# Performance work log

Measured on AMD Instinct MI355X. Metric: run time of the kernel, lower is better.

## Reference

```python
import math
import jax, jax.numpy as jnp
import numpy as np

D_HIDDEN, D_MODEL, SEQ_LEN = 2048, 4096, 4096
R_MIN, R_MAX, MAX_PHASE = 0.0, 1.0, 6.28


def setup_inputs() -> dict:
    key = jax.random.key(0)
    ks = jax.random.split(key, 8)
    # nu_log / theta_log per the LRU stable-ring init
    u1 = jax.random.uniform(ks[0], (D_HIDDEN,))
    nu_log = jnp.log(-0.5 * jnp.log(u1 * (R_MAX ** 2 - R_MIN ** 2) + R_MIN ** 2))
    u2 = jax.random.uniform(ks[1], (D_HIDDEN,))
    theta_log = jnp.log(MAX_PHASE * u2)
    diag_lambda = jnp.exp(-jnp.exp(nu_log) + 1j * jnp.exp(theta_log))
    gamma_log = jnp.log(jnp.sqrt(1.0 - jnp.abs(diag_lambda) ** 2))
    B_re = jax.random.normal(ks[2], (D_HIDDEN, D_MODEL)) / math.sqrt(2 * D_MODEL)
    B_im = jax.random.normal(ks[3], (D_HIDDEN, D_MODEL)) / math.sqrt(2 * D_MODEL)
    C_re = jax.random.normal(ks[4], (D_MODEL, D_HIDDEN)) / math.sqrt(D_HIDDEN)
    C_im = jax.random.normal(ks[5], (D_MODEL, D_HIDDEN)) / math.sqrt(D_HIDDEN)
    D = jax.random.normal(ks[6], (D_MODEL,))
    inputs = jax.random.normal(ks[7], (SEQ_LEN, D_MODEL), dtype=jnp.float32)
    return {
        "inputs": inputs,
        "nu_log": nu_log,
        "theta_log": theta_log,
        "gamma_log": gamma_log,
        "B_re": B_re,
        "B_im": B_im,
        "C_re": C_re,
        "C_im": C_im,
        "D": D,
    }


def reference(inputs, nu_log, theta_log, gamma_log, B_re, B_im, C_re, C_im, D):
    x = inputs.astype(jnp.complex64)
    # Diagonal complex recurrence matrix
    diag_lambda = jnp.exp(-jnp.exp(nu_log) + 1j * jnp.exp(theta_log))  # (H,)
    B_norm = (B_re + 1j * B_im) * jnp.exp(gamma_log)[:, None]          # (H, D)
    Bu = jnp.einsum('hd,td->th', B_norm, x)                            # (T, H)
    Lam = jnp.broadcast_to(diag_lambda, Bu.shape)                       # (T, H)

    # h_t = lambda * h_{t-1} + Bu_t  via log-depth associative scan
    def op(a, b):
        return (a[0] * b[0], b[0] * a[1] + b[1])

    _, hidden = jax.lax.associative_scan(op, (Lam, Bu))                 # (T, H)

    C = C_re + 1j * C_im                                                # (D, H)
    outputs = jnp.matmul(hidden, C.T).real + inputs * D                 # (T, D)
    return outputs.astype(jnp.float32)
```

## Files before the change

kernel.cpp:

```cpp
#include <hip/hip_runtime.h>
#include <hip/hip_bf16.h>

typedef unsigned short u16;
typedef float f32x4 __attribute__((ext_vector_type(4)));
typedef __bf16 bf16x8 __attribute__((ext_vector_type(8)));

constexpr int TSEQ = 4096;
constexpr int DMOD = 4096;
constexpr int HID  = 2048;
constexpr int HID2 = 4096;
constexpr int NCH  = 64;
constexpr int CHL  = 64;

__device__ __forceinline__ u16 f2bf(float f) {
  unsigned u = __builtin_bit_cast(unsigned, f);
  u += 0x7fffu + ((u >> 16) & 1u);
  return (u16)(u >> 16);
}
__device__ __forceinline__ float bf2f(u16 u) {
  return __builtin_bit_cast(float, (unsigned)u << 16);
}
__device__ __forceinline__ unsigned pack2(float a, float b) {
  return (unsigned)f2bf(a) | ((unsigned)f2bf(b) << 16);
}
__device__ __forceinline__ void load_lds16(const u16* g, u16* l) {
  __builtin_amdgcn_global_load_lds((const __attribute__((address_space(1))) void*)g,
                                   (__attribute__((address_space(3))) void*)l,
                                   16, 0, 0);
}
__device__ __forceinline__ unsigned lds_addr(const u16* p) {
  return (unsigned)(uintptr_t)(const __attribute__((address_space(3))) u16*)p;
}

__global__ __launch_bounds__(256) void k_lambda(const float* __restrict__ nu_log,
                                                const float* __restrict__ theta_log,
                                                float* __restrict__ lam_re, float* __restrict__ lam_im,
                                                float* __restrict__ lamL_re, float* __restrict__ lamL_im) {
  int h = blockIdx.x * 256 + threadIdx.x;
  if (h >= HID) return;
  float nu = expf(nu_log[h]);
  float th = expf(theta_log[h]);
  float mag = expf(-nu);
  float lr = mag * cosf(th), li = mag * sinf(th);
  lam_re[h] = lr; lam_im[h] = li;
  float pr = lr, pi = li;
#pragma unroll
  for (int i = 0; i < 6; ++i) {
    float nr = pr * pr - pi * pi;
    float ni = 2.f * pr * pi;
    pr = nr; pi = ni;
  }
  lamL_re[h] = pr; lamL_im[h] = pi;
}

__global__ __launch_bounds__(256) void k_cast_x(const float* __restrict__ x, u16* __restrict__ xb) {
  size_t i = ((size_t)blockIdx.x * 256 + threadIdx.x) * 4;
  float4 v = *reinterpret_cast<const float4*>(x + i);
  uint2 o;
  o.x = pack2(v.x, v.y);
  o.y = pack2(v.z, v.w);
  *reinterpret_cast<uint2*>(xb + i) = o;
}

__global__ __launch_bounds__(256) void k_make_bcat(const float* __restrict__ Bre, const float* __restrict__ Bim,
                                                   const float* __restrict__ gamma_log, u16* __restrict__ Bcat) {
  int idx = blockIdx.x * 256 + threadIdx.x;
  int h  = idx / (DMOD / 4);
  int dv = (idx % (DMOD / 4)) * 4;
  float g = expf(gamma_log[h]);
  float4 r  = *reinterpret_cast<const float4*>(Bre + (size_t)h * DMOD + dv);
  float4 im = *reinterpret_cast<const float4*>(Bim + (size_t)h * DMOD + dv);
  uint2 orr; orr.x = pack2(r.x * g, r.y * g); orr.y = pack2(r.z * g, r.w * g);
  *reinterpret_cast<uint2*>(Bcat + (size_t)h * DMOD + dv) = orr;
  uint2 oim; oim.x = pack2(im.x * g, im.y * g); oim.y = pack2(im.z * g, im.w * g);
  *reinterpret_cast<uint2*>(Bcat + (size_t)(h + HID) * DMOD + dv) = oim;
}

__global__ __launch_bounds__(256) void k_make_ccat(const float* __restrict__ Cre, const float* __restrict__ Cim,
                                                   u16* __restrict__ Ccat) {
  int idx = blockIdx.x * 256 + threadIdx.x;
  int d  = idx / (HID / 4);
  int hv = (idx % (HID / 4)) * 4;
  float4 r  = *reinterpret_cast<const float4*>(Cre + (size_t)d * HID + hv);
  float4 im = *reinterpret_cast<const float4*>(Cim + (size_t)d * HID + hv);
  uint2 orr; orr.x = pack2(r.x, r.y); orr.y = pack2(r.z, r.w);
  *reinterpret_cast<uint2*>(Ccat + (size_t)d * HID2 + hv) = orr;
  uint2 oim; oim.x = pack2(-im.x, -im.y); oim.y = pack2(-im.z, -im.w);
  *reinterpret_cast<uint2*>(Ccat + (size_t)d * HID2 + HID + hv) = oim;
}

#define DSR(d, a, IMM) asm volatile("ds_read_b128 %0, %1 offset:" IMM : "=v"(d) : "v"(a))

#define RD_A(B, O0, O1, O2, O3) do { \
  DSR(af[0][0], aAk0[B], O0); DSR(af[0][1], aAk1[B], O0); \
  DSR(af[1][0], aAk0[B], O1); DSR(af[1][1], aAk1[B], O1); \
  DSR(af[2][0], aAk0[B], O2); DSR(af[2][1], aAk1[B], O2); \
  DSR(af[3][0], aAk0[B], O3); DSR(af[3][1], aAk1[B], O3); } while (0)

#define RD_B(B, DST, O0, O1) do { \
  DSR(DST[0][0], aBk0[B], O0); DSR(DST[0][1], aBk1[B], O0); \
  DSR(DST[1][0], aBk0[B], O1); DSR(DST[1][1], aBk1[B], O1); } while (0)

#define STAGE_A(b, h, kb) do { const u16* _s = stA + (size_t)(h) * 128 * 4096 + (kb); \
  load_lds16(_s, dA[b][h]); load_lds16(_s + 64 * 4096, dA[b][h] + 4096); } while (0)
#define STAGE_B(b, h, kb) do { const u16* _s = stB + (size_t)(h) * 128 * 4096 + (kb); \
  load_lds16(_s, dB[b][h]); load_lds16(_s + 64 * 4096, dB[b][h] + 4096); } while (0)

#define MMQ(MB, NB, BF) do { \
  _Pragma("unroll") for (int k = 0; k < 2; ++k) { \
  _Pragma("unroll") for (int m = 0; m < 4; ++m) { \
  _Pragma("unroll") for (int n = 0; n < 2; ++n) { \
    acc[(MB)+m][(NB)+n] = __builtin_amdgcn_mfma_f32_16x16x32_bf16(af[m][k], BF[n][k], acc[(MB)+m][(NB)+n], 0, 0, 0); } } } } while (0)

#define MID() do { __builtin_amdgcn_s_barrier(); \
  asm volatile("s_waitcnt lgkmcnt(0)"); \
  __builtin_amdgcn_sched_barrier(0); \
  __builtin_amdgcn_s_setprio(1); } while (0)
#define ENDP() do { __builtin_amdgcn_s_setprio(0); \
  __builtin_amdgcn_s_barrier(); } while (0)
#define ENDPV() do { __builtin_amdgcn_s_setprio(0); \
  asm volatile("s_waitcnt vmcnt(4)"); \
  __builtin_amdgcn_s_barrier(); } while (0)

template <bool EPI>
__global__ __launch_bounds__(512, 2) void gemm8(const u16* __restrict__ A, const u16* __restrict__ Bt,
                                                void* __restrict__ Cout,
                                                const float* __restrict__ resid,
                                                const float* __restrict__ dvec) {
  constexpr int K = 4096, N = 4096;
  constexpr int NI = (K / 64) / 2;
  __shared__ __align__(16) u16 L[65536];

  int nwg = gridDim.x;
  int wg = blockIdx.x;
  wg = (wg & 7) * (nwg >> 3) + (wg >> 3);
  int bm = (wg >> 4) << 8;
  int bn = (wg & 15) << 8;

  int tid = threadIdx.x;
  int lane = tid & 63;
  int wave = tid >> 6;
  int wm = wave >> 2, wn = wave & 3;
  int l15 = lane & 15, g = lane >> 4;

  unsigned offk0 = (unsigned)(((unsigned)g << 4) ^ ((unsigned)(lane & 7) << 4));
  unsigned offk1 = offk0 ^ 64u;
  unsigned aAk0[2], aAk1[2], aBk0[2], aBk1[2];
#pragma unroll
  for (int b = 0; b < 2; ++b) {
    unsigned ab = lds_addr(&L[b * 32768 + wm * 8192 + l15 * 64]);
    aAk0[b] = ab + offk0; aAk1[b] = ab + offk1;
    unsigned bb = lds_addr(&L[b * 32768 + 16384 + (wn >> 1) * 8192 + (wn & 1) * 4096 + l15 * 64]);
    aBk0[b] = bb + offk0; aBk1[b] = bb + offk1;
  }

  int trow = tid >> 3;
  int tchk = ((tid & 7) ^ (trow & 7)) << 3;
  const u16* stA = A  + (size_t)(bm + trow) * K + tchk;
  const u16* stB = Bt + (size_t)(bn + trow) * K + tchk;
  u16* dA[2][2]; u16* dB[2][2];
#pragma unroll
  for (int b = 0; b < 2; ++b)
#pragma unroll
    for (int h = 0; h < 2; ++h) {
      dA[b][h] = &L[b * 32768 + h * 8192 + tid * 8];
      dB[b][h] = &L[b * 32768 + 16384 + h * 8192 + tid * 8];
    }

  bf16x8 af[4][2], b0[2][2], b1[2][2];
  f32x4 acc[8][4];
#pragma unroll
  for (int i = 0; i < 8; ++i)
#pragma unroll
    for (int n = 0; n < 4; ++n) acc[i][n] = (f32x4){0.f, 0.f, 0.f, 0.f};

  STAGE_B(0, 0, 0);  STAGE_A(0, 0, 0);
  STAGE_B(0, 1, 0);  STAGE_A(0, 1, 0);
  STAGE_B(1, 0, 64); STAGE_A(1, 0, 64);
  asm volatile("s_waitcnt vmcnt(4)");
  __builtin_amdgcn_s_barrier();

#pragma unroll 1
  for (int j = 0; j < NI; ++j) {
    int kb1 = ((2 * j + 1) << 6) & (K - 1);
    int kb2 = ((2 * j + 2) << 6) & (K - 1);
    int kb3 = ((2 * j + 3) << 6) & (K - 1);
    RD_A(0, "0", "2048", "4096", "6144");
    RD_B(0, b0, "0", "2048");
    STAGE_B(1, 1, kb1);
    MID(); MMQ(0, 0, b0); ENDP();
    RD_B(0, b1, "4096", "6144");
    STAGE_A(1, 1, kb1);
    MID(); MMQ(0, 2, b1); ENDP();
    RD_A(0, "8192", "10240", "12288", "14336");
    STAGE_B(0, 0, kb2);
    MID(); MMQ(4, 2, b1); ENDP();
    STAGE_A(0, 0, kb2);
    MID(); MMQ(4, 0, b0); ENDPV();
    RD_A(1, "0", "2048", "4096", "6144");
    RD_B(1, b0, "0", "2048");
    STAGE_B(0, 1, kb2);
    MID(); MMQ(0, 0, b0); ENDP();
    RD_B(1, b1, "4096", "6144");
    STAGE_A(0, 1, kb2);
    MID(); MMQ(0, 2, b1); ENDP();
    RD_A(1, "8192", "10240", "12288", "14336");
    STAGE_B(1, 0, kb3);
    MID(); MMQ(4, 2, b1); ENDP();
    STAGE_A(1, 0, kb3);
    MID(); MMQ(4, 0, b0); ENDPV();
  }

  int crow = bm + wm * 128 + (g << 2);
  int ccol = bn + wn * 64 + l15;
#pragma unroll
  for (int mi = 0; mi < 8; ++mi)
#pragma unroll
    for (int ni = 0; ni < 4; ++ni)
#pragma unroll
      for (int jj = 0; jj < 4; ++jj) {
        int row = crow + mi * 16 + jj;
        int col = ccol + ni * 16;
        float v = acc[mi][ni][jj];
        if constexpr (EPI) {
          v += resid[(size_t)row * N + col] * dvec[col];
          ((float*)Cout)[(size_t)row * N + col] = v;
        } else {
          ((u16*)Cout)[(size_t)row * N + col] = f2bf(v);
        }
      }
}

__global__ __launch_bounds__(256) void s_chunk_end(const u16* __restrict__ Bu,
                                                   const float* __restrict__ lam_re,
                                                   const float* __restrict__ lam_im,
                                                   float* __restrict__ E) {
  int t = blockIdx.x * 256 + threadIdx.x;
  int hq = t & (HID / 4 - 1);
  int c  = t >> 9;
  int h0 = hq << 2;
  float4 lr = *reinterpret_cast<const float4*>(lam_re + h0);
  float4 li = *reinterpret_cast<const float4*>(lam_im + h0);
  float sr[4] = {0.f, 0.f, 0.f, 0.f}, si[4] = {0.f, 0.f, 0.f, 0.f};
  const float lrv[4] = {lr.x, lr.y, lr.z, lr.w};
  const float liv[4] = {li.x, li.y, li.z, li.w};
  const u16* base = Bu + (size_t)c * CHL * HID2 + h0;
#pragma unroll 8
  for (int i = 0; i < CHL; ++i) {
    ushort4 vre = *reinterpret_cast<const ushort4*>(base + (size_t)i * HID2);
    ushort4 vim = *reinterpret_cast<const ushort4*>(base + (size_t)i * HID2 + HID);
    float br[4] = {bf2f(vre.x), bf2f(vre.y), bf2f(vre.z), bf2f(vre.w)};
    float bi[4] = {bf2f(vim.x), bf2f(vim.y), bf2f(vim.z), bf2f(vim.w)};
#pragma unroll
    for (int q = 0; q < 4; ++q) {
      float nr = lrv[q] * sr[q] - liv[q] * si[q] + br[q];
      float ni = lrv[q] * si[q] + liv[q] * sr[q] + bi[q];
      sr[q] = nr; si[q] = ni;
    }
  }
  *reinterpret_cast<float4*>(E + (size_t)c * HID + h0) = (float4){sr[0], sr[1], sr[2], sr[3]};
  *reinterpret_cast<float4*>(E + (size_t)NCH * HID + (size_t)c * HID + h0) = (float4){si[0], si[1], si[2], si[3]};
}

__global__ __launch_bounds__(256) void s_prefix(const float* __restrict__ lamL_re,
                                                const float* __restrict__ lamL_im,
                                                const float* __restrict__ E,
                                                float* __restrict__ P) {
  int h = blockIdx.x * 256 + threadIdx.x;
  if (h >= HID) return;
  float plr = lamL_re[h], pli = lamL_im[h];
  float pr = 0.f, pi = 0.f;
#pragma unroll
  for (int c = 0; c < NCH; ++c) {
    P[(size_t)c * HID + h] = pr;
    P[(size_t)NCH * HID + (size_t)c * HID + h] = pi;
    float er = E[(size_t)c * HID + h];
    float ei = E[(size_t)NCH * HID + (size_t)c * HID + h];
    float nr = plr * pr - pli * pi + er;
    float ni = plr * pi + pli * pr + ei;
    pr = nr; pi = ni;
  }
}

__global__ __launch_bounds__(256) void s_expand(const u16* __restrict__ Bu,
                                                const float* __restrict__ lam_re,
                                                const float* __restrict__ lam_im,
                                                const float* __restrict__ P,
                                                u16* __restrict__ A2) {
  int t = blockIdx.x * 256 + threadIdx.x;
  int hq = t & (HID / 4 - 1);
  int c  = t >> 9;
  int h0 = hq << 2;
  float4 lr = *reinterpret_cast<const float4*>(lam_re + h0);
  float4 li = *reinterpret_cast<const float4*>(lam_im + h0);
  const float lrv[4] = {lr.x, lr.y, lr.z, lr.w};
  const float liv[4] = {li.x, li.y, li.z, li.w};
  float4 p0 = *reinterpret_cast<const float4*>(P + (size_t)c * HID + h0);
  float4 p1 = *reinterpret_cast<const float4*>(P + (size_t)NCH * HID + (size_t)c * HID + h0);
  float sr[4] = {p0.x, p0.y, p0.z, p0.w}, si[4] = {p1.x, p1.y, p1.z, p1.w};
  const u16* base = Bu + (size_t)c * CHL * HID2 + h0;
  u16* ob = A2 + (size_t)c * CHL * HID2 + h0;
#pragma unroll 8
  for (int i = 0; i < CHL; ++i) {
    ushort4 vre = *reinterpret_cast<const ushort4*>(base + (size_t)i * HID2);
    ushort4 vim = *reinterpret_cast<const ushort4*>(base + (size_t)i * HID2 + HID);
    float br[4] = {bf2f(vre.x), bf2f(vre.y), bf2f(vre.z), bf2f(vre.w)};
    float bi[4] = {bf2f(vim.x), bf2f(vim.y), bf2f(vim.z), bf2f(vim.w)};
#pragma unroll
    for (int q = 0; q < 4; ++q) {
      float nr = lrv[q] * sr[q] - liv[q] * si[q] + br[q];
      float ni = lrv[q] * si[q] + liv[q] * sr[q] + bi[q];
      sr[q] = nr; si[q] = ni;
    }
    ushort4 ore = {f2bf(sr[0]), f2bf(sr[1]), f2bf(sr[2]), f2bf(sr[3])};
    ushort4 oim = {f2bf(si[0]), f2bf(si[1]), f2bf(si[2]), f2bf(si[3])};
    *reinterpret_cast<ushort4*>(ob + (size_t)i * HID2) = ore;
    *reinterpret_cast<ushort4*>(ob + (size_t)i * HID2 + HID) = oim;
  }
}

extern "C" void kernel_launch(void* const* d_in, const int* in_sizes, int n_in,
                              void* d_out, int out_size, void* d_ws, size_t ws_size,
                              hipStream_t stream) {
  const float* inputs    = (const float*)d_in[0];
  const float* nu_log    = (const float*)d_in[1];
  const float* theta_log = (const float*)d_in[2];
  const float* gamma_log = (const float*)d_in[3];
  const float* B_re      = (const float*)d_in[4];
  const float* B_im      = (const float*)d_in[5];
  const float* C_re      = (const float*)d_in[6];
  const float* C_im      = (const float*)d_in[7];
  const float* Dvec      = (const float*)d_in[8];

  char* w = (char*)d_ws;
  u16* xb     = (u16*)w;
  u16* Bcat   = (u16*)(w + (size_t)33554432);
  float* lam_re  = (float*)(w + (size_t)67108864);
  float* lam_im  = lam_re + HID;
  float* lamL_re = lam_im + HID;
  float* lamL_im = lamL_re + HID;
  float* E       = lamL_im + HID;
  float* P       = E + (size_t)NCH * HID * 2;

  u16* Bu    = (u16*)d_out;
  float* out = (float*)d_out;

  k_lambda<<<dim3(HID / 256), dim3(256), 0, stream>>>(nu_log, theta_log, lam_re, lam_im, lamL_re, lamL_im);
  k_cast_x<<<dim3((TSEQ * DMOD / 4) / 256), dim3(256), 0, stream>>>(inputs, xb);
  k_make_bcat<<<dim3((HID * DMOD / 4) / 256), dim3(256), 0, stream>>>(B_re, B_im, gamma_log, Bcat);

  gemm8<false><<<dim3((TSEQ / 256) * (HID2 / 256)), dim3(512), 0, stream>>>(
      xb, Bcat, (void*)Bu, nullptr, nullptr);

  s_chunk_end<<<dim3(NCH * HID / 4 / 256), dim3(256), 0, stream>>>(Bu, lam_re, lam_im, E);
  s_prefix<<<dim3(HID / 256), dim3(256), 0, stream>>>(lamL_re, lamL_im, E, P);
  s_expand<<<dim3(NCH * HID / 4 / 256), dim3(256), 0, stream>>>(Bu, lam_re, lam_im, P, xb );

  k_make_ccat<<<dim3((DMOD * HID / 4) / 256), dim3(256), 0, stream>>>(C_re, C_im, Bcat );

  gemm8<true><<<dim3((TSEQ / 256) * (DMOD / 256)), dim3(512), 0, stream>>>(
      xb , Bcat , (void*)out, inputs, Dvec);
}
```

Before: 478.8 us.

## Shorten scan chunks, widen scan parallelism, and double-buffer GEMM A fragments

```diff
diff --git a/kernel.cpp b/kernel.cpp
--- a/kernel.cpp
+++ b/kernel.cpp
@@ -9,8 +9,8 @@
 constexpr int DMOD = 4096;
 constexpr int HID  = 2048;
 constexpr int HID2 = 4096;
-constexpr int NCH  = 64;
-constexpr int CHL  = 64;
+constexpr int NCH  = 128;
+constexpr int CHL  = 32;
 
 __device__ __forceinline__ u16 f2bf(float f) {
   unsigned u = __builtin_bit_cast(unsigned, f);
@@ -45,7 +45,7 @@
   lam_re[h] = lr; lam_im[h] = li;
   float pr = lr, pi = li;
 #pragma unroll
-  for (int i = 0; i < 6; ++i) {
+  for (int i = 0; i < 5; ++i) {
     float nr = pr * pr - pi * pi;
     float ni = 2.f * pr * pi;
     pr = nr; pi = ni;
@@ -91,11 +91,11 @@
 
 #define DSR(d, a, IMM) asm volatile("ds_read_b128 %0, %1 offset:" IMM : "=v"(d) : "v"(a))
 
-#define RD_A(B, O0, O1, O2, O3) do { \
-  DSR(af[0][0], aAk0[B], O0); DSR(af[0][1], aAk1[B], O0); \
-  DSR(af[1][0], aAk0[B], O1); DSR(af[1][1], aAk1[B], O1); \
-  DSR(af[2][0], aAk0[B], O2); DSR(af[2][1], aAk1[B], O2); \
-  DSR(af[3][0], aAk0[B], O3); DSR(af[3][1], aAk1[B], O3); } while (0)
+#define RD_A(AF, B, O0, O1, O2, O3) do { \
+  DSR(AF[0][0], aAk0[B], O0); DSR(AF[0][1], aAk1[B], O0); \
+  DSR(AF[1][0], aAk0[B], O1); DSR(AF[1][1], aAk1[B], O1); \
+  DSR(AF[2][0], aAk0[B], O2); DSR(AF[2][1], aAk1[B], O2); \
+  DSR(AF[3][0], aAk0[B], O3); DSR(AF[3][1], aAk1[B], O3); } while (0)
 
 #define RD_B(B, DST, O0, O1) do { \
   DSR(DST[0][0], aBk0[B], O0); DSR(DST[0][1], aBk1[B], O0); \
@@ -106,14 +106,14 @@
 #define STAGE_B(b, h, kb) do { const u16* _s = stB + (size_t)(h) * 128 * 4096 + (kb); \
   load_lds16(_s, dB[b][h]); load_lds16(_s + 64 * 4096, dB[b][h] + 4096); } while (0)
 
-#define MMQ(MB, NB, BF) do { \
+#define MMQ(AF, MB, NB, BF) do { \
   _Pragma("unroll") for (int k = 0; k < 2; ++k) { \
   _Pragma("unroll") for (int m = 0; m < 4; ++m) { \
   _Pragma("unroll") for (int n = 0; n < 2; ++n) { \
-    acc[(MB)+m][(NB)+n] = __builtin_amdgcn_mfma_f32_16x16x32_bf16(af[m][k], BF[n][k], acc[(MB)+m][(NB)+n], 0, 0, 0); } } } } while (0)
-
-#define MID() do { __builtin_amdgcn_s_barrier(); \
-  asm volatile("s_waitcnt lgkmcnt(0)"); \
+    acc[(MB)+m][(NB)+n] = __builtin_amdgcn_mfma_f32_16x16x32_bf16(AF[m][k], BF[n][k], acc[(MB)+m][(NB)+n], 0, 0, 0); } } } } while (0)
+
+#define MIDN(CNT) do { __builtin_amdgcn_s_barrier(); \
+  asm volatile("s_waitcnt lgkmcnt(" CNT ")"); \
   __builtin_amdgcn_sched_barrier(0); \
   __builtin_amdgcn_s_setprio(1); } while (0)
 #define ENDP() do { __builtin_amdgcn_s_setprio(0); \
@@ -167,7 +167,7 @@
       dB[b][h] = &L[b * 32768 + 16384 + h * 8192 + tid * 8];
     }
 
-  bf16x8 af[4][2], b0[2][2], b1[2][2];
+  bf16x8 af1[4][2], af2[4][2], b0[2][2], b1[2][2];
   f32x4 acc[8][4];
 #pragma unroll
   for (int i = 0; i < 8; ++i)
@@ -185,30 +185,30 @@
     int kb1 = ((2 * j + 1) << 6) & (K - 1);
     int kb2 = ((2 * j + 2) << 6) & (K - 1);
     int kb3 = ((2 * j + 3) << 6) & (K - 1);
-    RD_A(0, "0", "2048", "4096", "6144");
+    RD_A(af1, 0, "0", "2048", "4096", "6144");
     RD_B(0, b0, "0", "2048");
+    RD_B(0, b1, "4096", "6144");
     STAGE_B(1, 1, kb1);
-    MID(); MMQ(0, 0, b0); ENDP();
-    RD_B(0, b1, "4096", "6144");
+    MIDN("4"); MMQ(af1, 0, 0, b0); ENDP();
+    RD_A(af2, 0, "8192", "10240", "12288", "14336");
     STAGE_A(1, 1, kb1);
-    MID(); MMQ(0, 2, b1); ENDP();
-    RD_A(0, "8192", "10240", "12288", "14336");
+    MIDN("8"); MMQ(af1, 0, 2, b1); ENDP();
     STAGE_B(0, 0, kb2);
-    MID(); MMQ(4, 2, b1); ENDP();
+    MIDN("0"); MMQ(af2, 4, 2, b1); ENDP();
     STAGE_A(0, 0, kb2);
-    MID(); MMQ(4, 0, b0); ENDPV();
-    RD_A(1, "0", "2048", "4096", "6144");
+    MIDN("0"); MMQ(af2, 4, 0, b0); ENDPV();
+    RD_A(af1, 1, "0", "2048", "4096", "6144");
     RD_B(1, b0, "0", "2048");
+    RD_B(1, b1, "4096", "6144");
     STAGE_B(0, 1, kb2);
-    MID(); MMQ(0, 0, b0); ENDP();
-    RD_B(1, b1, "4096", "6144");
+    MIDN("4"); MMQ(af1, 0, 0, b0); ENDP();
+    RD_A(af2, 1, "8192", "10240", "12288", "14336");
     STAGE_A(0, 1, kb2);
-    MID(); MMQ(0, 2, b1); ENDP();
-    RD_A(1, "8192", "10240", "12288", "14336");
+    MIDN("8"); MMQ(af1, 0, 2, b1); ENDP();
     STAGE_B(1, 0, kb3);
-    MID(); MMQ(4, 2, b1); ENDP();
+    MIDN("0"); MMQ(af2, 4, 2, b1); ENDP();
     STAGE_A(1, 0, kb3);
-    MID(); MMQ(4, 0, b0); ENDPV();
+    MIDN("0"); MMQ(af2, 4, 0, b0); ENDPV();
   }
 
   int crow = bm + wm * 128 + (g << 2);
@@ -236,30 +236,25 @@
                                                    const float* __restrict__ lam_im,
                                                    float* __restrict__ E) {
   int t = blockIdx.x * 256 + threadIdx.x;
-  int hq = t & (HID / 4 - 1);
-  int c  = t >> 9;
-  int h0 = hq << 2;
-  float4 lr = *reinterpret_cast<const float4*>(lam_re + h0);
-  float4 li = *reinterpret_cast<const float4*>(lam_im + h0);
-  float sr[4] = {0.f, 0.f, 0.f, 0.f}, si[4] = {0.f, 0.f, 0.f, 0.f};
-  const float lrv[4] = {lr.x, lr.y, lr.z, lr.w};
-  const float liv[4] = {li.x, li.y, li.z, li.w};
+  int hp = t & (HID / 2 - 1);
+  int c  = t >> 10;
+  int h0 = hp << 1;
+  float2 lr = *reinterpret_cast<const float2*>(lam_re + h0);
+  float2 li = *reinterpret_cast<const float2*>(lam_im + h0);
+  float sr0 = 0.f, si0 = 0.f, sr1 = 0.f, si1 = 0.f;
   const u16* base = Bu + (size_t)c * CHL * HID2 + h0;
 #pragma unroll 8
   for (int i = 0; i < CHL; ++i) {
-    ushort4 vre = *reinterpret_cast<const ushort4*>(base + (size_t)i * HID2);
-    ushort4 vim = *reinterpret_cast<const ushort4*>(base + (size_t)i * HID2 + HID);
-    float br[4] = {bf2f(vre.x), bf2f(vre.y), bf2f(vre.z), bf2f(vre.w)};
-    float bi[4] = {bf2f(vim.x), bf2f(vim.y), bf2f(vim.z), bf2f(vim.w)};
-#pragma unroll
-    for (int q = 0; q < 4; ++q) {
-      float nr = lrv[q] * sr[q] - liv[q] * si[q] + br[q];
-      float ni = lrv[q] * si[q] + liv[q] * sr[q] + bi[q];
-      sr[q] = nr; si[q] = ni;
-    }
-  }
-  *reinterpret_cast<float4*>(E + (size_t)c * HID + h0) = (float4){sr[0], sr[1], sr[2], sr[3]};
-  *reinterpret_cast<float4*>(E + (size_t)NCH * HID + (size_t)c * HID + h0) = (float4){si[0], si[1], si[2], si[3]};
+    ushort2 vre = *reinterpret_cast<const ushort2*>(base + (size_t)i * HID2);
+    ushort2 vim = *reinterpret_cast<const ushort2*>(base + (size_t)i * HID2 + HID);
+    float nr0 = lr.x * sr0 - li.x * si0 + bf2f(vre.x);
+    float ni0 = lr.x * si0 + li.x * sr0 + bf2f(vim.x);
+    float nr1 = lr.y * sr1 - li.y * si1 + bf2f(vre.y);
+    float ni1 = lr.y * si1 + li.y * sr1 + bf2f(vim.y);
+    sr0 = nr0; si0 = ni0; sr1 = nr1; si1 = ni1;
+  }
+  *reinterpret_cast<float2*>(E + (size_t)c * HID + h0) = (float2){sr0, sr1};
+  *reinterpret_cast<float2*>(E + (size_t)NCH * HID + (size_t)c * HID + h0) = (float2){si0, si1};
 }
 
 __global__ __launch_bounds__(256) void s_prefix(const float* __restrict__ lamL_re,
@@ -270,7 +265,7 @@
   if (h >= HID) return;
   float plr = lamL_re[h], pli = lamL_im[h];
   float pr = 0.f, pi = 0.f;
-#pragma unroll
+#pragma unroll 8
   for (int c = 0; c < NCH; ++c) {
     P[(size_t)c * HID + h] = pr;
     P[(size_t)NCH * HID + (size_t)c * HID + h] = pi;
@@ -288,34 +283,27 @@
                                                 const float* __restrict__ P,
                                                 u16* __restrict__ A2) {
   int t = blockIdx.x * 256 + threadIdx.x;
-  int hq = t & (HID / 4 - 1);
-  int c  = t >> 9;
-  int h0 = hq << 2;
-  float4 lr = *reinterpret_cast<const float4*>(lam_re + h0);
-  float4 li = *reinterpret_cast<const float4*>(lam_im + h0);
-  const float lrv[4] = {lr.x, lr.y, lr.z, lr.w};
-  const float liv[4] = {li.x, li.y, li.z, li.w};
-  float4 p0 = *reinterpret_cast<const float4*>(P + (size_t)c * HID + h0);
-  float4 p1 = *reinterpret_cast<const float4*>(P + (size_t)NCH * HID + (size_t)c * HID + h0);
-  float sr[4] = {p0.x, p0.y, p0.z, p0.w}, si[4] = {p1.x, p1.y, p1.z, p1.w};
+  int hp = t & (HID / 2 - 1);
+  int c  = t >> 10;
+  int h0 = hp << 1;
+  float2 lr = *reinterpret_cast<const float2*>(lam_re + h0);
+  float2 li = *reinterpret_cast<const float2*>(lam_im + h0);
+  float2 p0 = *reinterpret_cast<const float2*>(P + (size_t)c * HID + h0);
+  float2 p1 = *reinterpret_cast<const float2*>(P + (size_t)NCH * HID + (size_t)c * HID + h0);
+  float sr0 = p0.x, sr1 = p0.y, si0 = p1.x, si1 = p1.y;
   const u16* base = Bu + (size_t)c * CHL * HID2 + h0;
   u16* ob = A2 + (size_t)c * CHL * HID2 + h0;
 #pragma unroll 8
   for (int i = 0; i < CHL; ++i) {
-    ushort4 vre = *reinterpret_cast<const ushort4*>(base + (size_t)i * HID2);
-    ushort4 vim = *reinterpret_cast<const ushort4*>(base + (size_t)i * HID2 + HID);
-    float br[4] = {bf2f(vre.x), bf2f(vre.y), bf2f(vre.z), bf2f(vre.w)};
-    float bi[4] = {bf2f(vim.x), bf2f(vim.y), bf2f(vim.z), bf2f(vim.w)};
-#pragma unroll
-    for (int q = 0; q < 4; ++q) {
-      float nr = lrv[q] * sr[q] - liv[q] * si[q] + br[q];
-      float ni = lrv[q] * si[q] + liv[q] * sr[q] + bi[q];
-      sr[q] = nr; si[q] = ni;
-    }
-    ushort4 ore = {f2bf(sr[0]), f2bf(sr[1]), f2bf(sr[2]), f2bf(sr[3])};
-    ushort4 oim = {f2bf(si[0]), f2bf(si[1]), f2bf(si[2]), f2bf(si[3])};
-    *reinterpret_cast<ushort4*>(ob + (size_t)i * HID2) = ore;
-    *reinterpret_cast<ushort4*>(ob + (size_t)i * HID2 + HID) = oim;
+    ushort2 vre = *reinterpret_cast<const ushort2*>(base + (size_t)i * HID2);
+    ushort2 vim = *reinterpret_cast<const ushort2*>(base + (size_t)i * HID2 + HID);
+    float nr0 = lr.x * sr0 - li.x * si0 + bf2f(vre.x);
+    float ni0 = lr.x * si0 + li.x * sr0 + bf2f(vim.x);
+    float nr1 = lr.y * sr1 - li.y * si1 + bf2f(vre.y);
+    float ni1 = lr.y * si1 + li.y * sr1 + bf2f(vim.y);
+    sr0 = nr0; si0 = ni0; sr1 = nr1; si1 = ni1;
+    *reinterpret_cast<ushort2*>(ob + (size_t)i * HID2)       = (ushort2){f2bf(sr0), f2bf(sr1)};
+    *reinterpret_cast<ushort2*>(ob + (size_t)i * HID2 + HID) = (ushort2){f2bf(si0), f2bf(si1)};
   }
 }
 
@@ -339,11 +327,11 @@
   float* lam_im  = lam_re + HID;
   float* lamL_re = lam_im + HID;
   float* lamL_im = lamL_re + HID;
-  float* E       = lamL_im + HID;
-  float* P       = E + (size_t)NCH * HID * 2;
 
   u16* Bu    = (u16*)d_out;
   float* out = (float*)d_out;
+  float* E = (float*)((char*)d_out + (size_t)40 * 1024 * 1024);
+  float* P = (float*)((char*)d_out + (size_t)44 * 1024 * 1024);
 
   k_lambda<<<dim3(HID / 256), dim3(256), 0, stream>>>(nu_log, theta_log, lam_re, lam_im, lamL_re, lamL_im);
   k_cast_x<<<dim3((TSEQ * DMOD / 4) / 256), dim3(256), 0, stream>>>(inputs, xb);
@@ -352,9 +340,9 @@
   gemm8<false><<<dim3((TSEQ / 256) * (HID2 / 256)), dim3(512), 0, stream>>>(
       xb, Bcat, (void*)Bu, nullptr, nullptr);
 
-  s_chunk_end<<<dim3(NCH * HID / 4 / 256), dim3(256), 0, stream>>>(Bu, lam_re, lam_im, E);
+  s_chunk_end<<<dim3(NCH * HID / 2 / 256), dim3(256), 0, stream>>>(Bu, lam_re, lam_im, E);
   s_prefix<<<dim3(HID / 256), dim3(256), 0, stream>>>(lamL_re, lamL_im, E, P);
-  s_expand<<<dim3(NCH * HID / 4 / 256), dim3(256), 0, stream>>>(Bu, lam_re, lam_im, P, xb );
+  s_expand<<<dim3(NCH * HID / 2 / 256), dim3(256), 0, stream>>>(Bu, lam_re, lam_im, P, xb );
 
   k_make_ccat<<<dim3((DMOD * HID / 4) / 256), dim3(256), 0, stream>>>(C_re, C_im, Bcat );
 
```

New measurement: 492.3 us. +2.8%, slower.
